# Kernel tuning notes

Measured on AMD Instinct MI355X. Metric: run time of the kernel, lower is better.

Reference implementation:

```python
import jax, jax.numpy as jnp
import numpy as np
from jax import lax

# config: B=8, T=32, input_chans=1, H=kernel_size=8, W=n_freq=256
# F1=32, F2=48, F3=256, F4=128, n_note=88, pooling_size=2, filter_size3=(3,64)
B, T, CIN, H, W = 8, 32, 1, 8, 256
F1, F2, F3, F4, NNOTE = 32, 48, 256, 128, 88


def _conv2d(x, w, b, padding):
    # x: (B, Cin, H, W), w: (Cout, Cin, kh, kw)
    y = lax.conv_general_dilated(x, w, (1, 1), padding,
                                 dimension_numbers=('NCHW', 'OIHW', 'NCHW'))
    return y + b[None, :, None, None]


def _clstm(x, w, b, F):
    # x: (B, C, T, H, W); ConvLSTM (no peephole, no LN), 'same' padding.
    xs = jnp.moveaxis(x, 2, 0)  # (T, B, C, H, W)
    h0 = jnp.zeros((x.shape[0], F, x.shape[3], x.shape[4]), x.dtype)
    c0 = h0

    def step(carry, xt):
        h, c = carry
        z = _conv2d(jnp.concatenate([xt, h], axis=1), w, b, 'SAME')
        i, f, g, o = jnp.split(z, 4, axis=1)
        c = jax.nn.sigmoid(f) * c + jax.nn.sigmoid(i) * jnp.tanh(g)
        h = jax.nn.sigmoid(o) * jnp.tanh(c)
        return (h, c), h

    _, hs = lax.scan(step, (h0, c0), xs)  # (T, B, F, H, W)
    return jnp.moveaxis(hs, 0, 2)  # (B, F, T, H, W)


def _maxpool3d(x):
    # MaxPool3d(kernel=2, stride=2) over (T, H, W) of a (B, C, T, H, W) tensor
    return lax.reduce_window(x, -jnp.inf, lax.max,
                             (1, 1, 2, 2, 2), (1, 1, 2, 2, 2), 'VALID')


def setup_inputs() -> dict:
    key = jax.random.key(0)
    ks = jax.random.split(key, 11)
    s = 0.05
    return {
        'x':  jax.random.normal(ks[0], (B, CIN, T, H, W), jnp.float32),
        'w1': jax.random.normal(ks[1], (4 * F1, CIN + F1, 3, 3), jnp.float32) * s,
        'b1': jnp.zeros((4 * F1,), jnp.float32),
        'w2': jax.random.normal(ks[2], (4 * F2, F1 + F2, 3, 3), jnp.float32) * s,
        'b2': jnp.zeros((4 * F2,), jnp.float32),
        'w3': jax.random.normal(ks[3], (F3, F2, 3, 64), jnp.float32) * s,
        'b3': jnp.zeros((F3,), jnp.float32),
        'w4': jax.random.normal(ks[4], (F4, F3, 1, 1), jnp.float32) * s,
        'b4': jnp.zeros((F4,), jnp.float32),
        'w5': jax.random.normal(ks[5], (NNOTE, F4, 1, 1), jnp.float32) * s,
        'b5': jnp.zeros((NNOTE,), jnp.float32),
    }


def reference(x, w1, b1, w2, b2, w3, b3, w4, b4, w5, b5):
    x = _clstm(x, w1, b1, F1)          # (B, F1, T, H, W)
    x = _maxpool3d(x)                  # (B, F1, T/2, H/2, W/2)
    x = _clstm(x, w2, b2, F2)          # (B, F2, T/2, H/2, W/2)
    x = _maxpool3d(x)                  # (B, F2, 8, 2, 64)
    x = x.reshape(B, F2, -1, 64)       # (B, F2, 16, 64), filter_size3[1]=64
    x = jax.nn.elu(_conv2d(x, w3, b3, 'VALID'))  # (B, F3, 14, 1); dropout=eval noop
    x = jax.nn.elu(_conv2d(x, w4, b4, 'VALID'))  # (B, F4, 14, 1)
    x = _conv2d(x, w5, b5, 'VALID')              # (B, 88, 14, 1)
    return x
```

## Files before the change

kernel.cpp:

```cpp
#include <hip/hip_runtime.h>
#include <math.h>


#define DEVINL static __device__ __forceinline__
typedef __attribute__((ext_vector_type(8))) short short8;
typedef __attribute__((ext_vector_type(4))) float f32x4;

#define PLANE_W3 2359296

DEVINL float sigm(float x) { return 1.0f / (1.0f + __expf(-x)); }
DEVINL float tanh_fast(float x) { return 1.0f - 2.0f / (__expf(2.0f * x) + 1.0f); }
DEVINL float elu(float x) { return x > 0.0f ? x : expm1f(x); }
DEVINL unsigned short bf16_rne(float v) {
    unsigned u = __float_as_uint(v);
    unsigned r = (u + 0x7FFF + ((u >> 16) & 1)) >> 16;
    return (unsigned short)r;
}
DEVINL float bf16_to_f(unsigned short h) { return __uint_as_float(((unsigned)h) << 16); }
DEVINL unsigned pack_hl(float v) {
    unsigned short hi = bf16_rne(v);
    unsigned short lo = bf16_rne(v - bf16_to_f(hi));
    return (unsigned)hi | ((unsigned)lo << 16);
}
DEVINL float upk(unsigned u) {
    return __uint_as_float(u << 16) + __uint_as_float(u & 0xffff0000u);
}

DEVINL void lstm1_body(
    int xq, int y, int b, int t,
    const unsigned* __restrict__ xpk, const unsigned short* __restrict__ w1F,
    const float* __restrict__ b1,
    const unsigned* __restrict__ hprev, const unsigned* __restrict__ hpool,
    unsigned* __restrict__ hout, float* __restrict__ c1,
    unsigned* __restrict__ p1pk)
{
    __shared__ __align__(16) unsigned short sBhi[34 * 128];
    __shared__ __align__(16) unsigned short sBlo[34 * 128];
    const int x0 = xq * 32;
    const int tid = threadIdx.x;

    if (((t & 1) == 0) && t >= 2 && (y & 1) == 1) {
        int tp = (t >> 1) - 1, yp = y >> 1;
        for (int e = tid; e < 512; e += 256) {
            int f = e >> 4, xl = e & 15;
            int xp = (x0 >> 1) + xl, gx = x0 + 2 * xl;
            int b0 = ((b * 32 + f) * 8 + (y - 1)) * 256 + gx;
            float m = upk(hpool[b0]);
            m = fmaxf(m, upk(hpool[b0 + 1]));
            m = fmaxf(m, upk(hpool[b0 + 256]));
            m = fmaxf(m, upk(hpool[b0 + 257]));
            m = fmaxf(m, upk(hprev[b0]));
            m = fmaxf(m, upk(hprev[b0 + 1]));
            m = fmaxf(m, upk(hprev[b0 + 256]));
            m = fmaxf(m, upk(hprev[b0 + 257]));
            p1pk[(((b * 32 + f) * 16 + tp) * 4 + yp) * 128 + xp] = pack_hl(m);
        }
    }

    for (int e = tid; e < 34 * 128; e += 256) {
        int lx = e % 34, kk = e / 34;
        unsigned u = 0;
        if (kk < 99) {
            int ci = kk / 3, dy = kk - ci * 3;
            int gy = y + dy - 1, gx = x0 + lx - 1;
            if (gy >= 0 && gy < 8 && gx >= 0 && gx < 256)
                u = (ci == 0) ? xpk[((b * 32 + t) * 8 + gy) * 256 + gx]
                              : hprev[((b * 32 + (ci - 1)) * 8 + gy) * 256 + gx];
        }
        int a16 = lx * 128 + (((kk >> 3) ^ (lx & 15)) << 3) + (kk & 7);
        sBhi[a16] = (unsigned short)u;
        sBlo[a16] = (unsigned short)(u >> 16);
    }
    __syncthreads();

    const int l = tid & 63;
    const int wv = __builtin_amdgcn_readfirstlane(tid >> 6);
    const int ln = l & 15, kg = l >> 4;
    f32x4 acc[2][2];
#pragma unroll
    for (int i = 0; i < 2; ++i)
#pragma unroll
        for (int j = 0; j < 2; ++j) acc[i][j] = (f32x4){0.f, 0.f, 0.f, 0.f};

#pragma unroll
    for (int kk = 0; kk < 4; ++kk) {
        short8 bh[2][3], bl[2][3];
#pragma unroll
        for (int ntl = 0; ntl < 2; ++ntl)
#pragma unroll
            for (int dx = 0; dx < 3; ++dx) {
                int lx = ntl * 16 + ln + dx;
                int slot = kk * 4 + kg;
                int boff = lx * 128 + ((slot ^ (lx & 15)) << 3);
                bh[ntl][dx] = *(const short8*)&sBhi[boff];
                bl[ntl][dx] = *(const short8*)&sBlo[boff];
            }
#pragma unroll
        for (int mtl = 0; mtl < 2; ++mtl)
#pragma unroll
            for (int dx = 0; dx < 3; ++dx) {
                int aoff = ((((dx * 8 + wv * 2 + mtl) * 4 + kk) * 4 + kg) * 16 + ln) * 8;
                short8 ah = *(const short8*)&w1F[aoff];
#pragma unroll
                for (int ntl = 0; ntl < 2; ++ntl) {
                    acc[mtl][ntl] = __builtin_amdgcn_mfma_f32_16x16x32_bf16(ah, bl[ntl][dx], acc[mtl][ntl], 0, 0, 0);
                    acc[mtl][ntl] = __builtin_amdgcn_mfma_f32_16x16x32_bf16(ah, bh[ntl][dx], acc[mtl][ntl], 0, 0, 0);
                }
            }
    }

#pragma unroll
    for (int mtl = 0; mtl < 2; ++mtl) {
        const int f = (wv * 2 + mtl) * 4 + kg;
        const float bi = b1[f], bff = b1[32 + f], bg = b1[64 + f], bo = b1[96 + f];
#pragma unroll
        for (int ntl = 0; ntl < 2; ++ntl) {
            f32x4 a = acc[mtl][ntl];
            int gidx = ((b * 32 + f) * 8 + y) * 256 + x0 + ntl * 16 + ln;
            float zi = a[0] + bi, zf = a[1] + bff, zg = a[2] + bg, zo = a[3] + bo;
            float cv = c1[gidx];
            float cn = sigm(zf) * cv + sigm(zi) * tanh_fast(zg);
            c1[gidx] = cn;
            hout[gidx] = pack_hl(sigm(zo) * tanh_fast(cn));
        }
    }
}

DEVINL void lstm2_body(
    int xq, int y, int b, int t,
    const unsigned* __restrict__ p1pk, const unsigned short* __restrict__ w2F,
    const float* __restrict__ b2,
    const unsigned* __restrict__ hprev, const unsigned* __restrict__ hpool,
    float* __restrict__ c2, unsigned* __restrict__ hout,
    unsigned short* __restrict__ p2hi, unsigned short* __restrict__ p2lo,
    const unsigned* __restrict__ h30, const unsigned* __restrict__ h31)
{
    __shared__ __align__(16) unsigned short sChi[18 * 256];
    __shared__ __align__(16) unsigned short sClo[18 * 256];
    const int x0 = xq * 16;
    const int tid = threadIdx.x;

    if (((t & 1) == 0) && t >= 2 && y < 2) {
        int tp = (t >> 1) - 1;
        for (int e = tid; e < 48 * 8; e += 256) {
            int f = e >> 3, xl = e & 7;
            int xp = xq * 8 + xl;
            int g0 = ((b * 48 + f) * 4 + y * 2) * 128 + xp * 2;
            float m = fmaxf(fmaxf(upk(hpool[g0]), upk(hpool[g0 + 1])),
                            fmaxf(upk(hpool[g0 + 128]), upk(hpool[g0 + 129])));
            m = fmaxf(m, fmaxf(fmaxf(upk(hprev[g0]), upk(hprev[g0 + 1])),
                               fmaxf(upk(hprev[g0 + 128]), upk(hprev[g0 + 129]))));
            int pi = ((b * 48 + f) * 16 + tp * 2 + y) * 64 + xp;
            unsigned pm = pack_hl(m);
            p2hi[pi] = (unsigned short)pm;
            p2lo[pi] = (unsigned short)(pm >> 16);
        }
    }

    for (int idx = tid; idx < 80 * 54; idx += 256) {
        int ci = idx / 54, rem = idx % 54;
        int dy = rem / 18, lx = rem % 18;
        int gy = y + dy - 1, gx = x0 + lx - 1;
        unsigned u = 0;
        if (gy >= 0 && gy < 4 && gx >= 0 && gx < 128) {
            if (ci < 32) {
                if (t == 15) {
                    int b0 = ((b * 32 + ci) * 8 + gy * 2) * 256 + gx * 2;
                    float m = upk(h30[b0]);
                    m = fmaxf(m, upk(h30[b0 + 1]));
                    m = fmaxf(m, upk(h30[b0 + 256]));
                    m = fmaxf(m, upk(h30[b0 + 257]));
                    m = fmaxf(m, upk(h31[b0]));
                    m = fmaxf(m, upk(h31[b0 + 1]));
                    m = fmaxf(m, upk(h31[b0 + 256]));
                    m = fmaxf(m, upk(h31[b0 + 257]));
                    u = pack_hl(m);
                } else {
                    u = p1pk[(((b * 32 + ci) * 16 + t) * 4 + gy) * 128 + gx];
                }
            } else {
                u = hprev[((b * 48 + (ci - 32)) * 4 + gy) * 128 + gx];
            }
        }
        int k = ci * 3 + dy;
        int a16 = lx * 256 + (((k >> 3) ^ (lx & 15)) << 3) + (k & 7);
        sChi[a16] = (unsigned short)u;
        sClo[a16] = (unsigned short)(u >> 16);
    }
    for (int e = tid; e < 18 * 16; e += 256) {
        int lx = e >> 4, k = 240 + (e & 15);
        int a16 = lx * 256 + (((k >> 3) ^ (lx & 15)) << 3) + (k & 7);
        sChi[a16] = 0;
        sClo[a16] = 0;
    }
    __syncthreads();

    const int l = tid & 63;
    const int wv = __builtin_amdgcn_readfirstlane(tid >> 6);
    const int ln = l & 15, kg = l >> 4;
    f32x4 acc[3] = {{0.f,0.f,0.f,0.f},{0.f,0.f,0.f,0.f},{0.f,0.f,0.f,0.f}};

#pragma unroll
    for (int kk = 0; kk < 8; ++kk) {
        short8 bh[3], bl[3];
#pragma unroll
        for (int dx = 0; dx < 3; ++dx) {
            int lx = ln + dx;
            int boff = lx * 256 + ((((kk << 2) + kg) ^ (lx & 15)) << 3);
            bh[dx] = *(const short8*)&sChi[boff];
            bl[dx] = *(const short8*)&sClo[boff];
        }
#pragma unroll
        for (int j = 0; j < 3; ++j) {
            int mt = wv * 3 + j;
#pragma unroll
            for (int dx = 0; dx < 3; ++dx) {
                int aoff = ((((dx * 12 + mt) * 8 + kk) * 4 + kg) * 16 + ln) * 8;
                short8 ah = *(const short8*)&w2F[aoff];
                acc[j] = __builtin_amdgcn_mfma_f32_16x16x32_bf16(ah, bl[dx], acc[j], 0, 0, 0);
                acc[j] = __builtin_amdgcn_mfma_f32_16x16x32_bf16(ah, bh[dx], acc[j], 0, 0, 0);
            }
        }
    }

    const int x = x0 + ln;
#pragma unroll
    for (int j = 0; j < 3; ++j) {
        int mt = wv * 3 + j;
        int f = mt * 4 + kg;
        float zi = acc[j][0] + b2[f];
        float zf = acc[j][1] + b2[48 + f];
        float zg = acc[j][2] + b2[96 + f];
        float zo = acc[j][3] + b2[144 + f];
        int gidx = ((b * 48 + f) * 4 + y) * 128 + x;
        float cv = c2[gidx];
        float cn = sigm(zf) * cv + sigm(zi) * tanh_fast(zg);
        c2[gidx] = cn;
        hout[gidx] = pack_hl(sigm(zo) * tanh_fast(cn));
    }
}

__global__ __launch_bounds__(256) void step_k(
    const unsigned* __restrict__ xpk, const unsigned short* __restrict__ w1F,
    const float* __restrict__ b1,
    const unsigned* __restrict__ hprev1, const unsigned* __restrict__ hpool1,
    unsigned* __restrict__ hout1, float* __restrict__ c1,
    unsigned* __restrict__ p1pk,
    const unsigned short* __restrict__ w2F, const float* __restrict__ b2,
    const unsigned* __restrict__ hprev2, const unsigned* __restrict__ hpool2,
    unsigned* __restrict__ hout2, float* __restrict__ c2,
    unsigned short* __restrict__ p2hi, unsigned short* __restrict__ p2lo,
    int t, int t2)
{
    int bid = blockIdx.x;
    if (gridDim.x == 768) {
        if (bid < 256) {
            lstm2_body(bid & 7, (bid >> 3) & 3, bid >> 5, t2,
                       p1pk, w2F, b2, hprev2, hpool2, c2, hout2, p2hi, p2lo,
                       hout1, hout1);
            return;
        }
        bid -= 256;
    }
    lstm1_body(bid & 7, (bid >> 3) & 7, bid >> 6, t,
               xpk, w1F, b1, hprev1, hpool1, hout1, c1, p1pk);
}

__global__ __launch_bounds__(256) void lstm2_k(
    const unsigned* __restrict__ p1pk, const unsigned short* __restrict__ w2F,
    const float* __restrict__ b2,
    const unsigned* __restrict__ hprev, const unsigned* __restrict__ hpool,
    float* __restrict__ c2, unsigned* __restrict__ hout,
    unsigned short* __restrict__ p2hi, unsigned short* __restrict__ p2lo,
    const unsigned* __restrict__ h30, const unsigned* __restrict__ h31, int t)
{
    int bid = blockIdx.x;
    lstm2_body(bid & 7, (bid >> 3) & 3, bid >> 5, t,
               p1pk, w2F, b2, hprev, hpool, c2, hout, p2hi, p2lo, h30, h31);
}

__global__ void pool2(const unsigned* __restrict__ hA, const unsigned* __restrict__ hB,
                      unsigned short* __restrict__ p2hi, unsigned short* __restrict__ p2lo,
                      int tp)
{
    int idx = blockIdx.x * 256 + threadIdx.x;
    if (idx >= 8 * 48 * 2 * 64) return;
    int xp = idx & 63;
    int t1 = idx >> 6;
    int yp = t1 & 1; t1 >>= 1;
    int f = t1 % 48, b = t1 / 48;
    float m = -INFINITY;
#pragma unroll
    for (int dy = 0; dy < 2; ++dy)
#pragma unroll
        for (int dx = 0; dx < 2; ++dx) {
            int g = ((b * 48 + f) * 4 + yp * 2 + dy) * 128 + xp * 2 + dx;
            m = fmaxf(m, fmaxf(upk(hA[g]), upk(hB[g])));
        }
    int pi = ((b * 48 + f) * 16 + tp * 2 + yp) * 64 + xp;
    unsigned pm = pack_hl(m);
    p2hi[pi] = (unsigned short)pm;
    p2lo[pi] = (unsigned short)(pm >> 16);
}

__global__ __launch_bounds__(256) void conv3_part(
    const unsigned short* __restrict__ p2hi, const unsigned short* __restrict__ p2lo,
    const unsigned short* __restrict__ w3F,
    float* __restrict__ part)
{
    __shared__ float sRed[4 * 7 * 256];
    const int mq = blockIdx.x, ck = blockIdx.y;
    const int tid = threadIdx.x;
    const int l = tid & 63;
    const int wv = __builtin_amdgcn_readfirstlane(tid >> 6);
    const int c = ck * 4 + wv;
    const int ln = l & 15, kg = l >> 4;

    int rowbase[7];
#pragma unroll
    for (int nt = 0; nt < 7; ++nt) {
        int col = nt * 16 + ln;
        int bi = col / 14, r = col % 14;
        rowbase[nt] = (bi * 48 + c) * 16 + r;
    }

    f32x4 acc[7];
#pragma unroll
    for (int nt = 0; nt < 7; ++nt) acc[nt] = (f32x4){0.f, 0.f, 0.f, 0.f};

#pragma unroll
    for (int kk = 0; kk < 6; ++kk) {
        int aoff = ((((mq * 48 + c) * 6 + kk) * 4 + kg) * 16 + ln) * 8;
        short8 ah = *(const short8*)&w3F[aoff];
        short8 al = *(const short8*)&w3F[PLANE_W3 + aoff];
        int s = kk * 4 + kg;
        int dr = s >> 3, w0 = (s & 7) * 8;
#pragma unroll
        for (int nt = 0; nt < 7; ++nt) {
            int boff = (rowbase[nt] + dr) * 64 + w0;
            short8 bh = *(const short8*)&p2hi[boff];
            short8 bl = *(const short8*)&p2lo[boff];
            acc[nt] = __builtin_amdgcn_mfma_f32_16x16x32_bf16(al, bh, acc[nt], 0, 0, 0);
            acc[nt] = __builtin_amdgcn_mfma_f32_16x16x32_bf16(ah, bl, acc[nt], 0, 0, 0);
            acc[nt] = __builtin_amdgcn_mfma_f32_16x16x32_bf16(ah, bh, acc[nt], 0, 0, 0);
        }
    }

#pragma unroll
    for (int nt = 0; nt < 7; ++nt)
        *(f32x4*)&sRed[wv * 1792 + nt * 256 + l * 4] = acc[nt];
    __syncthreads();

#pragma unroll
    for (int nt = 0; nt < 7; ++nt) {
        float s = sRed[nt * 256 + tid] + sRed[1792 + nt * 256 + tid] +
                  sRed[2 * 1792 + nt * 256 + tid] + sRed[3 * 1792 + nt * 256 + tid];
        int r16 = (tid >> 6) * 4 + (tid & 3);
        int m = mq * 16 + r16;
        int col = nt * 16 + ((tid >> 2) & 15);
        part[(ck * 256 + m) * 112 + col] = s;
    }
}

__global__ __launch_bounds__(256) void head(
    const float* __restrict__ part, const float* __restrict__ b3,
    const float* __restrict__ w4T, const float* __restrict__ b4,
    const float* __restrict__ w5T, const float* __restrict__ b5,
    float* __restrict__ out)
{
    __shared__ float sO3[256];
    __shared__ float sO4[128];
    const int col = blockIdx.x;
    const int b = col / 14, r = col % 14;
    const int tid = threadIdx.x;

    float s = b3[tid];
#pragma unroll
    for (int ck = 0; ck < 12; ++ck)
        s += part[(ck * 256 + tid) * 112 + col];
    sO3[tid] = elu(s);
    __syncthreads();

    if (tid < 128) {
        float a4 = b4[tid];
        for (int c = 0; c < 256; ++c)
            a4 = fmaf(sO3[c], w4T[c * 128 + tid], a4);
        sO4[tid] = elu(a4);
    }
    __syncthreads();

    if (tid < 88) {
        float a5 = b5[tid];
        for (int c = 0; c < 128; ++c)
            a5 = fmaf(sO4[c], w5T[c * 88 + tid], a5);
        out[(b * 88 + tid) * 14 + r] = a5;
    }
}

__global__ void prep(const float* __restrict__ x, const float* __restrict__ w1,
                     const float* __restrict__ w2, const float* __restrict__ w3,
                     const float* __restrict__ w4, const float* __restrict__ w5,
                     unsigned* __restrict__ zeroA,
                     unsigned* __restrict__ zeroB,
                     unsigned* __restrict__ xpk,
                     unsigned short* __restrict__ w1F, unsigned short* __restrict__ w2F,
                     unsigned short* __restrict__ w3F,
                     float* __restrict__ w4T, float* __restrict__ w5T)
{
    int i = blockIdx.x * 256 + threadIdx.x;
    if (i < 65536) {
        uint4 z = {0, 0, 0, 0};
        uint4* p = (uint4*)&zeroA[i * 16];
        p[0] = z; p[1] = z; p[2] = z; p[3] = z;
        return;
    }
    i -= 65536;
    if (i < 24576) {
        uint4 z = {0, 0, 0, 0};
        uint4* p = (uint4*)&zeroB[i * 16];
        p[0] = z; p[1] = z; p[2] = z; p[3] = z;
        return;
    }
    i -= 24576;
    if (i < 131072) {
        const float4 v = *(const float4*)&x[i * 4];
        uint4 o;
        o.x = pack_hl(v.x); o.y = pack_hl(v.y);
        o.z = pack_hl(v.z); o.w = pack_hl(v.w);
        *(uint4*)&xpk[i * 4] = o;
        return;
    }
    i -= 131072;
    if (i < 6144) {
        int base = i * 8;
        int dx = base / 16384, rem = base % 16384;
        int mt = rem / 2048, r2 = rem % 2048;
        int kk = r2 / 512, r3 = r2 % 512;
        int kg = r3 / 128, ln = (r3 % 128) / 8;
        int f = mt * 4 + (ln >> 2), gate = ln & 3;
        int co = gate * 32 + f;
        int k0 = kk * 32 + kg * 8;
        short8 h;
#pragma unroll
        for (int e = 0; e < 8; ++e) {
            int k = k0 + e;
            float v = (k < 99) ? w1[co * 297 + (k / 3) * 9 + (k % 3) * 3 + dx] : 0.0f;
            h[e] = (short)bf16_rne(v);
        }
        *(short8*)&w1F[base] = h;
        return;
    }
    i -= 6144;
    if (i < 18432) {
        int base = i * 8;
        int dx = base / 49152, rem = base % 49152;
        int mt = rem / 4096, r2 = rem % 4096;
        int kk = r2 / 512, r3 = r2 % 512;
        int kg = r3 / 128, ln = (r3 % 128) / 8;
        int f = mt * 4 + (ln >> 2), gate = ln & 3;
        int co = gate * 48 + f;
        int k0 = kk * 32 + kg * 8;
        short8 h;
#pragma unroll
        for (int e = 0; e < 8; ++e) {
            int k = k0 + e;
            float v = (k < 240) ? w2[co * 720 + (k / 3) * 9 + (k % 3) * 3 + dx] : 0.0f;
            h[e] = (short)bf16_rne(v);
        }
        *(short8*)&w2F[base] = h;
        return;
    }
    i -= 18432;
    if (i < 294912) {
        int base = i * 8;
        int mq = base / 147456, rem = base % 147456;
        int c = rem / 3072, r2 = rem % 3072;
        int kk = r2 / 512, r3 = r2 % 512;
        int kg = r3 / 128, ln = (r3 % 128) / 8;
        int m = mq * 16 + ln;
        int kc0 = kk * 32 + kg * 8;
        int dr = kc0 >> 6, w0 = kc0 & 63;
        const float* src = &w3[((m * 48 + c) * 3 + dr) * 64 + w0];
        short8 hh, hl;
#pragma unroll
        for (int e = 0; e < 8; ++e) {
            float v = src[e];
            unsigned short hi = bf16_rne(v);
            hh[e] = (short)hi;
            hl[e] = (short)bf16_rne(v - bf16_to_f(hi));
        }
        *(short8*)&w3F[base] = hh;
        *(short8*)&w3F[PLANE_W3 + base] = hl;
        return;
    }
    i -= 294912;
    if (i < 32768) {
        int n = i / 256, cch = i % 256;
        w4T[cch * 128 + n] = w4[i];
        return;
    }
    i -= 32768;
    if (i < 11264) {
        int n = i / 128, cch = i % 128;
        w5T[cch * 88 + n] = w5[i];
    }
}

extern "C" void kernel_launch(void* const* d_in, const int* in_sizes, int n_in,
                              void* d_out, int out_size, void* d_ws, size_t ws_size,
                              hipStream_t stream)
{
    const float* x  = (const float*)d_in[0];
    const float* w1 = (const float*)d_in[1];
    const float* b1 = (const float*)d_in[2];
    const float* w2 = (const float*)d_in[3];
    const float* b2 = (const float*)d_in[4];
    const float* w3 = (const float*)d_in[5];
    const float* b3 = (const float*)d_in[6];
    const float* w4 = (const float*)d_in[7];
    const float* b4 = (const float*)d_in[8];
    const float* w5 = (const float*)d_in[9];
    const float* b5 = (const float*)d_in[10];
    float* out = (float*)d_out;

    float* ws = (float*)d_ws;
    size_t off = 0;
    auto alloc = [&](size_t n) { float* p = ws + off; off += n; return p; };
    unsigned* h1[3];
    h1[0] = (unsigned*)alloc(524288); h1[1] = (unsigned*)alloc(524288);
    h1[2] = (unsigned*)alloc(524288);
    float* c1 = alloc(524288);
    unsigned* xpk = (unsigned*)alloc(524288);
    unsigned* p1pk = (unsigned*)alloc(2097152);
    unsigned* h2[3];
    h2[0] = (unsigned*)alloc(196608); h2[1] = (unsigned*)alloc(196608);
    h2[2] = (unsigned*)alloc(196608);
    float* c2 = alloc(196608);
    unsigned short* p2hi = (unsigned short*)alloc(196608);
    unsigned short* p2lo = (unsigned short*)alloc(196608);
    float* part = alloc(344064);
    unsigned short* w1F = (unsigned short*)alloc(24576);
    unsigned short* w2F = (unsigned short*)alloc(73728);
    unsigned short* w3F = (unsigned short*)alloc(2359296);
    float* w4T = alloc(32768);
    float* w5T = alloc(11264);
    (void)ws_size; (void)off;

    prep<<<2284, 256, 0, stream>>>(x, w1, w2, w3, w4, w5,
                                   h1[2], h2[2], xpk, w1F, w2F, w3F, w4T, w5T);

    for (int t = 0; t < 32; ++t) {
        int t2 = ((t & 1) == 0 && t >= 4) ? (t - 4) / 2 : (t == 31 ? 14 : -1);
        int nblk = (t2 >= 0) ? 768 : 512;
        step_k<<<nblk, 256, 0, stream>>>(
            xpk, w1F, b1, h1[(t + 2) % 3], h1[(t + 1) % 3], h1[t % 3], c1, p1pk,
            w2F, b2,
            t2 >= 0 ? h2[(t2 + 2) % 3] : h2[0],
            t2 >= 0 ? h2[(t2 + 1) % 3] : h2[0],
            t2 >= 0 ? h2[t2 % 3] : h2[0],
            c2, p2hi, p2lo, t, t2);
    }

    lstm2_k<<<256, 256, 0, stream>>>(p1pk, w2F, b2, h2[2], h2[1], c2, h2[0],
                                     p2hi, p2lo, h1[0], h1[1], 15);
    pool2<<<192, 256, 0, stream>>>(h2[2], h2[0], p2hi, p2lo, 7);

    conv3_part<<<dim3(16, 12), 256, 0, stream>>>(p2hi, p2lo, w3F, part);
    head<<<112, 256, 0, stream>>>(part, b3, w4T, b4, w5T, b5, out);
}
```

Before: 484.6 us.

## Compute two LSTM1 timesteps per launch using halo recompute in LDS

Replaces the per-timestep LSTM1 kernel with a paired kernel where each block computes timestep 2j over a halo-extended 3x34 tile, keeps the resulting hidden state in LDS, then computes timestep 2j+1 for its 32-column tile without a global round trip. This halves the number of sequential launches in the recurrence and the associated global synchronisation. It also removes the prep-time zeroing and x packing by handling t=0 inline and packing x on the fly. The cost is redundant halo MFMA work, larger LDS use (about 45KB) and more accumulator registers, which may lower occupancy. The pooling schedule and LSTM2 tail launches are reorganised to match.

Result: slower. 1.078 ms (+122.4%).

```diff
diff --git a/kernel.cpp b/kernel.cpp
--- a/kernel.cpp
+++ b/kernel.cpp
@@ -26,106 +26,6 @@
     return __uint_as_float(u << 16) + __uint_as_float(u & 0xffff0000u);
 }
 
-DEVINL void lstm1_body(
-    int xq, int y, int b, int t,
-    const unsigned* __restrict__ xpk, const unsigned short* __restrict__ w1F,
-    const float* __restrict__ b1,
-    const unsigned* __restrict__ hprev, const unsigned* __restrict__ hpool,
-    unsigned* __restrict__ hout, float* __restrict__ c1,
-    unsigned* __restrict__ p1pk)
-{
-    __shared__ __align__(16) unsigned short sBhi[34 * 128];
-    __shared__ __align__(16) unsigned short sBlo[34 * 128];
-    const int x0 = xq * 32;
-    const int tid = threadIdx.x;
-
-    if (((t & 1) == 0) && t >= 2 && (y & 1) == 1) {
-        int tp = (t >> 1) - 1, yp = y >> 1;
-        for (int e = tid; e < 512; e += 256) {
-            int f = e >> 4, xl = e & 15;
-            int xp = (x0 >> 1) + xl, gx = x0 + 2 * xl;
-            int b0 = ((b * 32 + f) * 8 + (y - 1)) * 256 + gx;
-            float m = upk(hpool[b0]);
-            m = fmaxf(m, upk(hpool[b0 + 1]));
-            m = fmaxf(m, upk(hpool[b0 + 256]));
-            m = fmaxf(m, upk(hpool[b0 + 257]));
-            m = fmaxf(m, upk(hprev[b0]));
-            m = fmaxf(m, upk(hprev[b0 + 1]));
-            m = fmaxf(m, upk(hprev[b0 + 256]));
-            m = fmaxf(m, upk(hprev[b0 + 257]));
-            p1pk[(((b * 32 + f) * 16 + tp) * 4 + yp) * 128 + xp] = pack_hl(m);
-        }
-    }
-
-    for (int e = tid; e < 34 * 128; e += 256) {
-        int lx = e % 34, kk = e / 34;
-        unsigned u = 0;
-        if (kk < 99) {
-            int ci = kk / 3, dy = kk - ci * 3;
-            int gy = y + dy - 1, gx = x0 + lx - 1;
-            if (gy >= 0 && gy < 8 && gx >= 0 && gx < 256)
-                u = (ci == 0) ? xpk[((b * 32 + t) * 8 + gy) * 256 + gx]
-                              : hprev[((b * 32 + (ci - 1)) * 8 + gy) * 256 + gx];
-        }
-        int a16 = lx * 128 + (((kk >> 3) ^ (lx & 15)) << 3) + (kk & 7);
-        sBhi[a16] = (unsigned short)u;
-        sBlo[a16] = (unsigned short)(u >> 16);
-    }
-    __syncthreads();
-
-    const int l = tid & 63;
-    const int wv = __builtin_amdgcn_readfirstlane(tid >> 6);
-    const int ln = l & 15, kg = l >> 4;
-    f32x4 acc[2][2];
-#pragma unroll
-    for (int i = 0; i < 2; ++i)
-#pragma unroll
-        for (int j = 0; j < 2; ++j) acc[i][j] = (f32x4){0.f, 0.f, 0.f, 0.f};
-
-#pragma unroll
-    for (int kk = 0; kk < 4; ++kk) {
-        short8 bh[2][3], bl[2][3];
-#pragma unroll
-        for (int ntl = 0; ntl < 2; ++ntl)
-#pragma unroll
-            for (int dx = 0; dx < 3; ++dx) {
-                int lx = ntl * 16 + ln + dx;
-                int slot = kk * 4 + kg;
-                int boff = lx * 128 + ((slot ^ (lx & 15)) << 3);
-                bh[ntl][dx] = *(const short8*)&sBhi[boff];
-                bl[ntl][dx] = *(const short8*)&sBlo[boff];
-            }
-#pragma unroll
-        for (int mtl = 0; mtl < 2; ++mtl)
-#pragma unroll
-            for (int dx = 0; dx < 3; ++dx) {
-                int aoff = ((((dx * 8 + wv * 2 + mtl) * 4 + kk) * 4 + kg) * 16 + ln) * 8;
-                short8 ah = *(const short8*)&w1F[aoff];
-#pragma unroll
-                for (int ntl = 0; ntl < 2; ++ntl) {
-                    acc[mtl][ntl] = __builtin_amdgcn_mfma_f32_16x16x32_bf16(ah, bl[ntl][dx], acc[mtl][ntl], 0, 0, 0);
-                    acc[mtl][ntl] = __builtin_amdgcn_mfma_f32_16x16x32_bf16(ah, bh[ntl][dx], acc[mtl][ntl], 0, 0, 0);
-                }
-            }
-    }
-
-#pragma unroll
-    for (int mtl = 0; mtl < 2; ++mtl) {
-        const int f = (wv * 2 + mtl) * 4 + kg;
-        const float bi = b1[f], bff = b1[32 + f], bg = b1[64 + f], bo = b1[96 + f];
-#pragma unroll
-        for (int ntl = 0; ntl < 2; ++ntl) {
-            f32x4 a = acc[mtl][ntl];
-            int gidx = ((b * 32 + f) * 8 + y) * 256 + x0 + ntl * 16 + ln;
-            float zi = a[0] + bi, zf = a[1] + bff, zg = a[2] + bg, zo = a[3] + bo;
-            float cv = c1[gidx];
-            float cn = sigm(zf) * cv + sigm(zi) * tanh_fast(zg);
-            c1[gidx] = cn;
-            hout[gidx] = pack_hl(sigm(zo) * tanh_fast(cn));
-        }
-    }
-}
-
 DEVINL void lstm2_body(
     int xq, int y, int b, int t,
     const unsigned* __restrict__ p1pk, const unsigned short* __restrict__ w2F,
@@ -133,10 +33,9 @@
     const unsigned* __restrict__ hprev, const unsigned* __restrict__ hpool,
     float* __restrict__ c2, unsigned* __restrict__ hout,
     unsigned short* __restrict__ p2hi, unsigned short* __restrict__ p2lo,
-    const unsigned* __restrict__ h30, const unsigned* __restrict__ h31)
-{
-    __shared__ __align__(16) unsigned short sChi[18 * 256];
-    __shared__ __align__(16) unsigned short sClo[18 * 256];
+    const unsigned* __restrict__ h30, const unsigned* __restrict__ h31,
+    unsigned short* sChi, unsigned short* sClo)
+{
     const int x0 = xq * 16;
     const int tid = threadIdx.x;
 
@@ -178,7 +77,7 @@
                 } else {
                     u = p1pk[(((b * 32 + ci) * 16 + t) * 4 + gy) * 128 + gx];
                 }
-            } else {
+            } else if (t > 0) {
                 u = hprev[((b * 48 + (ci - 32)) * 4 + gy) * 128 + gx];
             }
         }
@@ -233,37 +132,219 @@
         float zg = acc[j][2] + b2[96 + f];
         float zo = acc[j][3] + b2[144 + f];
         int gidx = ((b * 48 + f) * 4 + y) * 128 + x;
-        float cv = c2[gidx];
+        float cv = (t > 0) ? c2[gidx] : 0.0f;
         float cn = sigm(zf) * cv + sigm(zi) * tanh_fast(zg);
         c2[gidx] = cn;
         hout[gidx] = pack_hl(sigm(zo) * tanh_fast(cn));
     }
 }
 
-__global__ __launch_bounds__(256) void step_k(
-    const unsigned* __restrict__ xpk, const unsigned short* __restrict__ w1F,
+DEVINL void lstm1_pair(
+    int xq, int y, int b, int j, int poolIdx,
+    const float* __restrict__ x, const unsigned short* __restrict__ w1F,
     const float* __restrict__ b1,
-    const unsigned* __restrict__ hprev1, const unsigned* __restrict__ hpool1,
-    unsigned* __restrict__ hout1, float* __restrict__ c1,
+    const unsigned* __restrict__ hprev,
+    const unsigned* __restrict__ hA, const unsigned* __restrict__ hB,
+    unsigned* __restrict__ hC, unsigned* __restrict__ hD,
+    const float* __restrict__ cPrev, float* __restrict__ cOut,
+    unsigned* __restrict__ p1pk,
+    unsigned short* rawHi, unsigned short* rawLo, float* cLds)
+{
+    const int x0 = xq * 32;
+    const int t0 = 2 * j;
+    const int tid = threadIdx.x;
+
+    if (j >= 1) {
+        int idx = poolIdx * 256 + tid;
+        int xp = idx & 127, q1 = idx >> 7;
+        int yp = q1 & 3, q2 = q1 >> 2;
+        int f = q2 & 31, bb = q2 >> 5;
+        int base = ((bb * 32 + f) * 8 + yp * 2) * 256 + xp * 2;
+        float m = upk(hA[base]);
+        m = fmaxf(m, upk(hA[base + 1]));
+        m = fmaxf(m, upk(hA[base + 256]));
+        m = fmaxf(m, upk(hA[base + 257]));
+        m = fmaxf(m, upk(hB[base]));
+        m = fmaxf(m, upk(hB[base + 1]));
+        m = fmaxf(m, upk(hB[base + 256]));
+        m = fmaxf(m, upk(hB[base + 257]));
+        p1pk[(((bb * 32 + f) * 16 + (j - 1)) * 4 + yp) * 128 + xp] = pack_hl(m);
+    }
+
+    for (int e = tid; e < 7200; e += 256) {
+        int lx = e % 36, r2 = e / 36;
+        int frow = r2 % 5, ci = r2 / 5;
+        int gy = y - 2 + frow, gx = x0 - 2 + lx;
+        unsigned u = 0;
+        if (ci < 33 && gy >= 0 && gy < 8 && gx >= 0 && gx < 256) {
+            if (ci == 0) u = pack_hl(x[((b * 32 + t0) * 8 + gy) * 256 + gx]);
+            else if (j > 0) u = hprev[((b * 32 + ci - 1) * 8 + gy) * 256 + gx];
+        }
+        int a = (frow * 36 + lx) * 40 + ci;
+        rawHi[a] = (unsigned short)u;
+        rawLo[a] = (unsigned short)(u >> 16);
+    }
+    __syncthreads();
+
+    const int l = tid & 63;
+    const int wv = __builtin_amdgcn_readfirstlane(tid >> 6);
+    const int mh = wv >> 1, nh = wv & 1;
+    const int ln = l & 15, kg = l >> 4;
+    const int ntB = nh * 4;
+
+    f32x4 acc[5][4];
+#pragma unroll
+    for (int i = 0; i < 5; ++i)
+#pragma unroll
+        for (int m2 = 0; m2 < 4; ++m2) acc[i][m2] = (f32x4){0.f, 0.f, 0.f, 0.f};
+
+#pragma unroll
+    for (int kk = 0; kk < 4; ++kk) {
+        int q = kk * 4 + kg;
+        int dy0 = (q >= 15) ? 2 : q / 5;
+        int ci0 = (q % 5) * 8;
+#pragma unroll
+        for (int dx = 0; dx < 3; ++dx) {
+            short8 bh[5], bl[5];
+#pragma unroll
+            for (int ntl = 0; ntl < 5; ++ntl) {
+                int nt = ntB + ntl;
+                int r = nt / 3, ct = nt - r * 3;
+                int lx = ct * 16 + ln + dx;
+                lx = (lx > 35) ? 35 : lx;
+                int a = ((r + dy0) * 36 + lx) * 40 + ci0;
+                bh[ntl] = *(const short8*)&rawHi[a];
+                bl[ntl] = *(const short8*)&rawLo[a];
+            }
+#pragma unroll
+            for (int mtl = 0; mtl < 4; ++mtl) {
+                int aoff = ((((dx * 8 + mh * 4 + mtl) * 4 + kk) * 4 + kg) * 16 + ln) * 8;
+                short8 ah = *(const short8*)&w1F[aoff];
+#pragma unroll
+                for (int ntl = 0; ntl < 5; ++ntl) {
+                    acc[ntl][mtl] = __builtin_amdgcn_mfma_f32_16x16x32_bf16(ah, bl[ntl], acc[ntl][mtl], 0, 0, 0);
+                    acc[ntl][mtl] = __builtin_amdgcn_mfma_f32_16x16x32_bf16(ah, bh[ntl], acc[ntl][mtl], 0, 0, 0);
+                }
+            }
+        }
+    }
+    __syncthreads();
+
+#pragma unroll
+    for (int mtl = 0; mtl < 4; ++mtl) {
+        const int f = (mh * 4 + mtl) * 4 + kg;
+        const float bi = b1[f], bff = b1[32 + f], bg = b1[64 + f], bo = b1[96 + f];
+#pragma unroll
+        for (int ntl = 0; ntl < 5; ++ntl) {
+            int nt = ntB + ntl;
+            int r = nt / 3, ct = nt - r * 3;
+            int cp = ct * 16 + ln;
+            if (cp < 34) {
+                int crel = cp - 1;
+                int grow = y - 1 + r;
+                int col = x0 + crel;
+                float hv = 0.0f, cn = 0.0f;
+                if (grow >= 0 && grow < 8 && col >= 0 && col < 256) {
+                    f32x4 a = acc[ntl][mtl];
+                    float zi = a[0] + bi, zf = a[1] + bff;
+                    float zg = a[2] + bg, zo = a[3] + bo;
+                    float cv = (j > 0) ? cPrev[((b * 32 + f) * 8 + grow) * 256 + col] : 0.0f;
+                    cn = sigm(zf) * cv + sigm(zi) * tanh_fast(zg);
+                    hv = sigm(zo) * tanh_fast(cn);
+                }
+                unsigned pk = pack_hl(hv);
+                int a2 = ((r + 1) * 36 + (crel + 2)) * 40 + 1 + f;
+                rawHi[a2] = (unsigned short)pk;
+                rawLo[a2] = (unsigned short)(pk >> 16);
+                if (r == 1 && crel >= 0 && crel < 32) {
+                    cLds[f * 32 + crel] = cn;
+                    hC[((b * 32 + f) * 8 + y) * 256 + col] = pk;
+                }
+            }
+        }
+    }
+
+    for (int e = tid; e < 102; e += 256) {
+        int lx = e % 34 + 1, frow = e / 34 + 1;
+        int gy = y - 2 + frow, gx = x0 - 2 + lx;
+        unsigned u = 0;
+        if (gy >= 0 && gy < 8 && gx >= 0 && gx < 256)
+            u = pack_hl(x[((b * 32 + t0 + 1) * 8 + gy) * 256 + gx]);
+        int a = (frow * 36 + lx) * 40;
+        rawHi[a] = (unsigned short)u;
+        rawLo[a] = (unsigned short)(u >> 16);
+    }
+    __syncthreads();
+
+    f32x4 acc2[4];
+#pragma unroll
+    for (int m2 = 0; m2 < 4; ++m2) acc2[m2] = (f32x4){0.f, 0.f, 0.f, 0.f};
+#pragma unroll
+    for (int kk = 0; kk < 4; ++kk) {
+        int q = kk * 4 + kg;
+        int dy0 = q / 5;
+        int ci0 = (q % 5) * 8;
+#pragma unroll
+        for (int dx = 0; dx < 3; ++dx) {
+            int lx = nh * 16 + ln + dx + 1;
+            int a = ((1 + dy0) * 36 + lx) * 40 + ci0;
+            short8 bh2 = *(const short8*)&rawHi[a];
+            short8 bl2 = *(const short8*)&rawLo[a];
+#pragma unroll
+            for (int mtl = 0; mtl < 4; ++mtl) {
+                int aoff = ((((dx * 8 + mh * 4 + mtl) * 4 + kk) * 4 + kg) * 16 + ln) * 8;
+                short8 ah = *(const short8*)&w1F[aoff];
+                acc2[mtl] = __builtin_amdgcn_mfma_f32_16x16x32_bf16(ah, bl2, acc2[mtl], 0, 0, 0);
+                acc2[mtl] = __builtin_amdgcn_mfma_f32_16x16x32_bf16(ah, bh2, acc2[mtl], 0, 0, 0);
+            }
+        }
+    }
+
+#pragma unroll
+    for (int mtl = 0; mtl < 4; ++mtl) {
+        const int f = (mh * 4 + mtl) * 4 + kg;
+        int col = x0 + nh * 16 + ln;
+        f32x4 a = acc2[mtl];
+        float zi = a[0] + b1[f], zf = a[1] + b1[32 + f];
+        float zg = a[2] + b1[64 + f], zo = a[3] + b1[96 + f];
+        float cv = cLds[f * 32 + nh * 16 + ln];
+        float cn = sigm(zf) * cv + sigm(zi) * tanh_fast(zg);
+        int g = ((b * 32 + f) * 8 + y) * 256 + col;
+        cOut[g] = cn;
+        hD[g] = pack_hl(sigm(zo) * tanh_fast(cn));
+    }
+}
+
+__global__ __launch_bounds__(256) void fused_k(
+    const float* __restrict__ x, const unsigned short* __restrict__ w1F,
+    const float* __restrict__ b1,
+    const unsigned* __restrict__ hprev, const unsigned* __restrict__ hA,
+    const unsigned* __restrict__ hB,
+    unsigned* __restrict__ hC, unsigned* __restrict__ hD,
+    const float* __restrict__ cPrev, float* __restrict__ cOut,
     unsigned* __restrict__ p1pk,
     const unsigned short* __restrict__ w2F, const float* __restrict__ b2,
-    const unsigned* __restrict__ hprev2, const unsigned* __restrict__ hpool2,
-    unsigned* __restrict__ hout2, float* __restrict__ c2,
+    const unsigned* __restrict__ h2prev, const unsigned* __restrict__ h2pool,
+    unsigned* __restrict__ h2out, float* __restrict__ c2,
     unsigned short* __restrict__ p2hi, unsigned short* __restrict__ p2lo,
-    int t, int t2)
-{
+    int j, int t2)
+{
+    __shared__ __align__(16) unsigned char lds[45184];
     int bid = blockIdx.x;
-    if (gridDim.x == 768) {
+    if (t2 >= 0) {
         if (bid < 256) {
             lstm2_body(bid & 7, (bid >> 3) & 3, bid >> 5, t2,
-                       p1pk, w2F, b2, hprev2, hpool2, c2, hout2, p2hi, p2lo,
-                       hout1, hout1);
+                       p1pk, w2F, b2, h2prev, h2pool, c2, h2out, p2hi, p2lo,
+                       hC, hC,
+                       (unsigned short*)lds, (unsigned short*)(lds + 9216));
             return;
         }
         bid -= 256;
     }
-    lstm1_body(bid & 7, (bid >> 3) & 7, bid >> 6, t,
-               xpk, w1F, b1, hprev1, hpool1, hout1, c1, p1pk);
+    lstm1_pair(bid & 7, (bid >> 3) & 7, bid >> 6, j, bid,
+               x, w1F, b1, hprev, hA, hB, hC, hD, cPrev, cOut, p1pk,
+               (unsigned short*)lds, (unsigned short*)(lds + 14400),
+               (float*)(lds + 28800));
 }
 
 __global__ __launch_bounds__(256) void lstm2_k(
@@ -274,9 +355,12 @@
     unsigned short* __restrict__ p2hi, unsigned short* __restrict__ p2lo,
     const unsigned* __restrict__ h30, const unsigned* __restrict__ h31, int t)
 {
+    __shared__ __align__(16) unsigned short sChi[18 * 256];
+    __shared__ __align__(16) unsigned short sClo[18 * 256];
     int bid = blockIdx.x;
     lstm2_body(bid & 7, (bid >> 3) & 3, bid >> 5, t,
-               p1pk, w2F, b2, hprev, hpool, c2, hout, p2hi, p2lo, h30, h31);
+               p1pk, w2F, b2, hprev, hpool, c2, hout, p2hi, p2lo, h30, h31,
+               sChi, sClo);
 }
 
 __global__ void pool2(const unsigned* __restrict__ hA, const unsigned* __restrict__ hB,
@@ -397,40 +481,14 @@
     }
 }
 
-__global__ void prep(const float* __restrict__ x, const float* __restrict__ w1,
-                     const float* __restrict__ w2, const float* __restrict__ w3,
-                     const float* __restrict__ w4, const float* __restrict__ w5,
-                     unsigned* __restrict__ zeroA,
-                     unsigned* __restrict__ zeroB,
-                     unsigned* __restrict__ xpk,
+__global__ void prep(const float* __restrict__ w1, const float* __restrict__ w2,
+                     const float* __restrict__ w3, const float* __restrict__ w4,
+                     const float* __restrict__ w5,
                      unsigned short* __restrict__ w1F, unsigned short* __restrict__ w2F,
                      unsigned short* __restrict__ w3F,
                      float* __restrict__ w4T, float* __restrict__ w5T)
 {
     int i = blockIdx.x * 256 + threadIdx.x;
-    if (i < 65536) {
-        uint4 z = {0, 0, 0, 0};
-        uint4* p = (uint4*)&zeroA[i * 16];
-        p[0] = z; p[1] = z; p[2] = z; p[3] = z;
-        return;
-    }
-    i -= 65536;
-    if (i < 24576) {
-        uint4 z = {0, 0, 0, 0};
-        uint4* p = (uint4*)&zeroB[i * 16];
-        p[0] = z; p[1] = z; p[2] = z; p[3] = z;
-        return;
-    }
-    i -= 24576;
-    if (i < 131072) {
-        const float4 v = *(const float4*)&x[i * 4];
-        uint4 o;
-        o.x = pack_hl(v.x); o.y = pack_hl(v.y);
-        o.z = pack_hl(v.z); o.w = pack_hl(v.w);
-        *(uint4*)&xpk[i * 4] = o;
-        return;
-    }
-    i -= 131072;
     if (i < 6144) {
         int base = i * 8;
         int dx = base / 16384, rem = base % 16384;
@@ -439,12 +497,15 @@
         int kg = r3 / 128, ln = (r3 % 128) / 8;
         int f = mt * 4 + (ln >> 2), gate = ln & 3;
         int co = gate * 32 + f;
-        int k0 = kk * 32 + kg * 8;
+        int q = kk * 4 + kg;
         short8 h;
 #pragma unroll
         for (int e = 0; e < 8; ++e) {
-            int k = k0 + e;
-            float v = (k < 99) ? w1[co * 297 + (k / 3) * 9 + (k % 3) * 3 + dx] : 0.0f;
+            float v = 0.0f;
+            if (q < 15) {
+                int dy = q / 5, ci = (q % 5) * 8 + e;
+                if (ci < 33) v = w1[co * 297 + ci * 9 + dy * 3 + dx];
+            }
             h[e] = (short)bf16_rne(v);
         }
         *(short8*)&w1F[base] = h;
@@ -526,11 +587,11 @@
     float* ws = (float*)d_ws;
     size_t off = 0;
     auto alloc = [&](size_t n) { float* p = ws + off; off += n; return p; };
-    unsigned* h1[3];
+    unsigned* h1[4];
     h1[0] = (unsigned*)alloc(524288); h1[1] = (unsigned*)alloc(524288);
-    h1[2] = (unsigned*)alloc(524288);
-    float* c1 = alloc(524288);
-    unsigned* xpk = (unsigned*)alloc(524288);
+    h1[2] = (unsigned*)alloc(524288); h1[3] = (unsigned*)alloc(524288);
+    float* c1[2];
+    c1[0] = alloc(524288); c1[1] = alloc(524288);
     unsigned* p1pk = (unsigned*)alloc(2097152);
     unsigned* h2[3];
     h2[0] = (unsigned*)alloc(196608); h2[1] = (unsigned*)alloc(196608);
@@ -546,24 +607,31 @@
     float* w5T = alloc(11264);
     (void)ws_size; (void)off;
 
-    prep<<<2284, 256, 0, stream>>>(x, w1, w2, w3, w4, w5,
-                                   h1[2], h2[2], xpk, w1F, w2F, w3F, w4T, w5T);
-
-    for (int t = 0; t < 32; ++t) {
-        int t2 = ((t & 1) == 0 && t >= 4) ? (t - 4) / 2 : (t == 31 ? 14 : -1);
+    prep<<<1420, 256, 0, stream>>>(w1, w2, w3, w4, w5, w1F, w2F, w3F, w4T, w5T);
+
+    for (int j = 0; j < 16; ++j) {
+        int t2 = j - 2;
         int nblk = (t2 >= 0) ? 768 : 512;
-        step_k<<<nblk, 256, 0, stream>>>(
-            xpk, w1F, b1, h1[(t + 2) % 3], h1[(t + 1) % 3], h1[t % 3], c1, p1pk,
-            w2F, b2,
+        fused_k<<<nblk, 256, 0, stream>>>(
+            x, w1F, b1,
+            h1[(2 * j + 3) & 3],
+            h1[(2 * j + 2) & 3],
+            h1[(2 * j + 3) & 3],
+            h1[(2 * j) & 3],
+            h1[(2 * j + 1) & 3],
+            c1[(j + 1) & 1], c1[j & 1],
+            p1pk, w2F, b2,
             t2 >= 0 ? h2[(t2 + 2) % 3] : h2[0],
             t2 >= 0 ? h2[(t2 + 1) % 3] : h2[0],
             t2 >= 0 ? h2[t2 % 3] : h2[0],
-            c2, p2hi, p2lo, t, t2);
-    }
-
-    lstm2_k<<<256, 256, 0, stream>>>(p1pk, w2F, b2, h2[2], h2[1], c2, h2[0],
-                                     p2hi, p2lo, h1[0], h1[1], 15);
-    pool2<<<192, 256, 0, stream>>>(h2[2], h2[0], p2hi, p2lo, 7);
+            c2, p2hi, p2lo, j, t2);
+    }
+
+    lstm2_k<<<256, 256, 0, stream>>>(p1pk, w2F, b2, h2[(14 + 2) % 3], h2[(14 + 1) % 3],
+                                     c2, h2[14 % 3], p2hi, p2lo, h1[0], h1[0], 14);
+    lstm2_k<<<256, 256, 0, stream>>>(p1pk, w2F, b2, h2[(15 + 2) % 3], h2[(15 + 1) % 3],
+                                     c2, h2[15 % 3], p2hi, p2lo, h1[2], h1[3], 15);
+    pool2<<<192, 256, 0, stream>>>(h2[14 % 3], h2[15 % 3], p2hi, p2lo, 7);
 
     conv3_part<<<dim3(16, 12), 256, 0, stream>>>(p2hi, p2lo, w3F, part);
     head<<<112, 256, 0, stream>>>(part, b3, w4T, b4, w5T, b5, out);
```
